# Optimization experiments

Hardware: AMD Instinct MI355X
Metric: run time of the kernel (lower is better)

The kernel has to match this reference:

```python
import jax, jax.numpy as jnp
import numpy as np

N_NODES = 100000
N_EDGES = 1600000
F_IN = 512
HID = 128
N_CLASS = 6


def setup_inputs() -> dict:
    key = jax.random.key(0)
    ks = jax.random.split(key, 12)
    def unif(k, shape, stdv):
        return jax.random.uniform(k, shape, jnp.float32, -stdv, stdv)
    s1 = 1.0 / np.sqrt(HID); s4 = 1.0 / np.sqrt(N_CLASS)
    return {
        "x": jax.random.normal(ks[0], (N_NODES, F_IN), jnp.float32),
        "edge_row": jax.random.randint(ks[1], (N_EDGES,), 0, N_NODES, jnp.int32),
        "edge_col": jax.random.randint(ks[2], (N_EDGES,), 0, N_NODES, jnp.int32),
        "edge_weight": jax.random.uniform(ks[3], (N_EDGES,), jnp.float32),
        "W1": unif(ks[4], (F_IN, HID), s1), "b1": unif(ks[5], (HID,), s1),
        "W2": unif(ks[6], (HID, HID), s1), "b2": unif(ks[7], (HID,), s1),
        "W3": unif(ks[8], (HID, HID), s1), "b3": unif(ks[9], (HID,), s1),
        "W4": unif(ks[10], (HID, N_CLASS), s4), "b4": unif(ks[11], (N_CLASS,), s4),
    }


def _gcn_layer(x, row, col, w_e, W, b):
    # support = x @ W  (dense mm), then spmm(adj, support) in COO form:
    # out[i] = sum_{(i,j) in E} A[i,j] * support[j]
    support = x @ W                              # [N, F_out]
    msgs = support[col] * w_e[:, None]           # [E, F_out] gather + scale
    agg = jax.ops.segment_sum(msgs, row, num_segments=N_NODES)
    return agg + b


def reference(x, edge_row, edge_col, edge_weight, W1, b1, W2, b2, W3, b3, W4, b4):
    # eval mode: F.dropout(training=False) is identity
    h = jax.nn.relu(_gcn_layer(x, edge_row, edge_col, edge_weight, W1, b1))
    h = jax.nn.relu(_gcn_layer(h, edge_row, edge_col, edge_weight, W2, b2))
    h = jax.nn.relu(_gcn_layer(h, edge_row, edge_col, edge_weight, W3, b3))
    return _gcn_layer(h, edge_row, edge_col, edge_weight, W4, b4)
```

## Files before the change

### kernel.cpp

```cpp
#include <hip/hip_runtime.h>
#include <cstdint>

constexpr int NN = 100000;
constexpr int NE = 1600000;
constexpr int FIN = 512;
constexpr int HID = 128;
constexpr int NCLS = 6;
constexpr int EPAD = NE + 3 * NN;

typedef __attribute__((ext_vector_type(8))) short short8v;
typedef __attribute__((ext_vector_type(4))) float f32x4;

constexpr float WINV = 1.0f / 32767.0f;

__device__ __forceinline__ unsigned short f2bf(float f) {
    uint32_t u = __float_as_uint(f);
    uint32_t r = u + 0x7FFFu + ((u >> 16) & 1u);
    return (unsigned short)(r >> 16);
}
__device__ __forceinline__ float bflo(uint32_t u) { return __uint_as_float(u << 16); }
__device__ __forceinline__ float bfhi(uint32_t u) { return __uint_as_float(u & 0xffff0000u); }

__device__ __forceinline__ void gl_lds16(const void* g, void* l) {
    __builtin_amdgcn_global_load_lds(
        (const __attribute__((address_space(1))) unsigned int*)(unsigned long long)g,
        (__attribute__((address_space(3))) unsigned int*)(unsigned int)(unsigned long long)l,
        16, 0, 0);
}

__device__ __forceinline__ void cvt_body(const float* __restrict__ W,
                                         unsigned short* __restrict__ Bp, int t) {
    const int lane = t & 63;
    const int fi = t >> 6;
    const int n = fi & 7, ks = fi >> 3;
    const int krow = ks * 32 + (lane >> 4) * 8;
    const int col = n * 16 + (lane & 15);
    short8v sv;
    #pragma unroll
    for (int j = 0; j < 8; ++j) sv[j] = (short)f2bf(W[(size_t)(krow + j) * HID + col]);
    *(short8v*)&Bp[(size_t)t * 8] = sv;
}

template<int K, bool ABF>
__device__ __forceinline__ void gemm_body(unsigned char* lds,
                                          const void* __restrict__ Av,
                                          const unsigned short* __restrict__ Bp,
                                          unsigned short* __restrict__ C, int bid) {
    constexpr int BM    = 160;
    constexpr int KS    = 32;
    constexpr int EB    = ABF ? 2 : 4;
    constexpr int ROWB  = KS * EB;
    constexpr int SLOTS = ROWB / 16;
    constexpr int SMSK  = SLOTS - 1;
    constexpr int CHUNK = BM * ROWB;
    constexpr int WBYT  = CHUNK / 5;
    constexpr int NISS  = WBYT / 1024;
    constexpr int NS    = K / KS;
    constexpr int WAITN = 8 + NISS;

    const int tid  = threadIdx.x;
    const int lane = tid & 63;
    const int wave = tid >> 6;
    const int row0 = bid * BM;
    const int lr   = lane & 15;
    const int kg   = lane >> 4;

    const unsigned char* Ab = (const unsigned char*)Av;
    const size_t rowbytes = (size_t)K * EB;

    auto stage = [&](int bufsel, int ks) {
        const size_t kbyte = (size_t)ks * ROWB;
        #pragma unroll
        for (int i = 0; i < NISS; ++i) {
            const int Lw   = wave * WBYT + i * 1024 + lane * 16;
            const int row  = Lw / ROWB;
            const int slot = (Lw >> 4) & SMSK;
            const int src  = slot ^ (row & SMSK);
            const unsigned char* g = Ab + (size_t)(row0 + row) * rowbytes + kbyte + src * 16;
            void* l = (void*)&lds[bufsel * CHUNK + wave * WBYT + i * 1024];
            gl_lds16(g, l);
        }
    };

    auto loadB = [&](int ks, short8v (&b)[8]) {
        const unsigned short* bb = Bp + ((size_t)ks * 8 * 64 + lane) * 8;
        #pragma unroll
        for (int n = 0; n < 8; ++n)
            b[n] = *reinterpret_cast<const short8v*>(bb + (size_t)n * 64 * 8);
    };

    short8v bcur[8], bnxt[8];
    f32x4 acc[2][8] = {};

    loadB(0, bcur);
    stage(0, 0);
    asm volatile("s_waitcnt vmcnt(0)" ::: "memory");
    __builtin_amdgcn_sched_barrier(0);

    int cur = 0;
    for (int ks = 0; ks < NS; ++ks) {
        if (ks + 1 < NS) {
            loadB(ks + 1, bnxt);
            stage(cur ^ 1, ks + 1);
            if (ks > 0) {
                asm volatile("s_waitcnt vmcnt(%0)" :: "i"(WAITN) : "memory");
            }
        } else {
            asm volatile("s_waitcnt vmcnt(0)" ::: "memory");
        }
        __builtin_amdgcn_sched_barrier(0);

        const unsigned char* base = &lds[cur * CHUNK];
        const int rA0 = wave * 32 + lr;
        const int rA1 = rA0 + 16;
        const int key = lr & SMSK;

        short8v a0, a1;
        if constexpr (ABF) {
            a0 = *(const short8v*)(base + rA0 * ROWB + ((kg ^ key) * 16));
            a1 = *(const short8v*)(base + rA1 * ROWB + ((kg ^ key) * 16));
        } else {
            const float4 f00 = *(const float4*)(base + rA0 * ROWB + (((2 * kg + 0) ^ key) * 16));
            const float4 f01 = *(const float4*)(base + rA0 * ROWB + (((2 * kg + 1) ^ key) * 16));
            const float4 f10 = *(const float4*)(base + rA1 * ROWB + (((2 * kg + 0) ^ key) * 16));
            const float4 f11 = *(const float4*)(base + rA1 * ROWB + (((2 * kg + 1) ^ key) * 16));
            a0[0] = (short)f2bf(f00.x); a0[1] = (short)f2bf(f00.y);
            a0[2] = (short)f2bf(f00.z); a0[3] = (short)f2bf(f00.w);
            a0[4] = (short)f2bf(f01.x); a0[5] = (short)f2bf(f01.y);
            a0[6] = (short)f2bf(f01.z); a0[7] = (short)f2bf(f01.w);
            a1[0] = (short)f2bf(f10.x); a1[1] = (short)f2bf(f10.y);
            a1[2] = (short)f2bf(f10.z); a1[3] = (short)f2bf(f10.w);
            a1[4] = (short)f2bf(f11.x); a1[5] = (short)f2bf(f11.y);
            a1[6] = (short)f2bf(f11.z); a1[7] = (short)f2bf(f11.w);
        }

        #pragma unroll
        for (int n = 0; n < 8; ++n) {
            acc[0][n] = __builtin_amdgcn_mfma_f32_16x16x32_bf16(a0, bcur[n], acc[0][n], 0, 0, 0);
            acc[1][n] = __builtin_amdgcn_mfma_f32_16x16x32_bf16(a1, bcur[n], acc[1][n], 0, 0, 0);
        }
        if (ks + 1 < NS) {
            #pragma unroll
            for (int n = 0; n < 8; ++n) bcur[n] = bnxt[n];
        }
        cur ^= 1;
    }

    #pragma unroll
    for (int m = 0; m < 2; ++m)
        #pragma unroll
        for (int n = 0; n < 8; ++n)
            #pragma unroll
            for (int i = 0; i < 4; ++i) {
                const int r = row0 + wave * 32 + m * 16 + kg * 4 + i;
                C[(size_t)r * HID + n * 16 + lr] = f2bf(acc[m][n][i]);
            }
}

__launch_bounds__(320)
__global__ void gemm_lds_bf(const void* __restrict__ Av, const unsigned short* __restrict__ Bp,
                            unsigned short* __restrict__ C) {
    __shared__ __attribute__((aligned(16))) unsigned char lds[2 * 160 * 64];
    gemm_body<HID, true>(lds, Av, Bp, C, blockIdx.x);
}

__device__ __forceinline__ void scatter_one(int r, int c, float w,
                                            const int* __restrict__ row_ptr,
                                            int* __restrict__ cur,
                                            uint32_t* __restrict__ edges) {
    const int pos = row_ptr[r] + atomicAdd(&cur[r], 1);
    edges[pos] = ((uint32_t)c << 15) | (uint32_t)(w * 32767.0f + 0.5f);
}

__global__ void fused_hist_cvt(const int4* __restrict__ erow4, int* __restrict__ cnt,
                               const float* __restrict__ W1, const float* __restrict__ W2,
                               const float* __restrict__ W3,
                               unsigned short* __restrict__ Bp1, unsigned short* __restrict__ Bp2,
                               unsigned short* __restrict__ Bp3) {
    constexpr int NB_HIST = (NE / 4 + 255) / 256;
    const int bid = blockIdx.x;
    if (bid < NB_HIST) {
        const int t = bid * 256 + threadIdx.x;
        if (t < NE / 4) {
            const int4 r = erow4[t];
            atomicAdd(&cnt[r.x], 1);
            atomicAdd(&cnt[r.y], 1);
            atomicAdd(&cnt[r.z], 1);
            atomicAdd(&cnt[r.w], 1);
        }
    } else {
        const int t = (bid - NB_HIST) * 256 + threadIdx.x;
        constexpr int T1 = (FIN / 32) * 8 * 64;
        constexpr int T2 = (HID / 32) * 8 * 64;
        if (t < T1)                cvt_body(W1, Bp1, t);
        else if (t < T1 + T2)      cvt_body(W2, Bp2, t - T1);
        else if (t < T1 + 2 * T2)  cvt_body(W3, Bp3, t - T1 - T2);
    }
}

constexpr int GB_GEMM = NN / 160;
constexpr int GB_SCAT = (NE / 4 + 319) / 320;
constexpr int GB_PAD  = (NN + 319) / 320;

__launch_bounds__(320)
__global__ void fused_l1(const float* __restrict__ x, const unsigned short* __restrict__ Bp1,
                         unsigned short* __restrict__ sup16,
                         const int4* __restrict__ erow4, const int4* __restrict__ ecol4,
                         const float4* __restrict__ ew4,
                         const int* __restrict__ row_ptr, const int* __restrict__ row_cnt,
                         int* __restrict__ cur, uint32_t* __restrict__ edges) {
    __shared__ __attribute__((aligned(16))) unsigned char lds[2 * 160 * 128];
    const int bid = blockIdx.x;
    if (bid < GB_GEMM) {
        gemm_body<FIN, false>(lds, x, Bp1, sup16, bid);
    } else if (bid < GB_GEMM + GB_SCAT) {
        const int t = (bid - GB_GEMM) * 320 + threadIdx.x;
        if (t < NE / 4) {
            const int4 r = erow4[t];
            const int4 c = ecol4[t];
            const float4 w = ew4[t];
            scatter_one(r.x, c.x, w.x, row_ptr, cur, edges);
            scatter_one(r.y, c.y, w.y, row_ptr, cur, edges);
            scatter_one(r.z, c.z, w.z, row_ptr, cur, edges);
            scatter_one(r.w, c.w, w.w, row_ptr, cur, edges);
        }
    } else {
        const int r = (bid - GB_GEMM - GB_SCAT) * 320 + threadIdx.x;
        if (r < NN) {
            const int end = row_ptr[r + 1];
            for (int p = row_ptr[r] + row_cnt[r]; p < end; ++p) edges[p] = 0u;
        }
    }
}

__global__ void gemm_w4(const unsigned short* __restrict__ H, const float* __restrict__ W,
                        float* __restrict__ S, int M) {
    __shared__ float Ws[HID * NCLS];
    for (int i = threadIdx.x; i < HID * NCLS; i += blockDim.x) Ws[i] = W[i];
    __syncthreads();
    const int r = blockIdx.x * blockDim.x + threadIdx.x;
    if (r >= M) return;
    float acc[NCLS] = {};
    const unsigned short* h = &H[(size_t)r * HID];
    for (int k0 = 0; k0 < HID; k0 += 8) {
        const uint4 hv = *reinterpret_cast<const uint4*>(&h[k0]);
        float hf[8];
        hf[0] = bflo(hv.x); hf[1] = bfhi(hv.x);
        hf[2] = bflo(hv.y); hf[3] = bfhi(hv.y);
        hf[4] = bflo(hv.z); hf[5] = bfhi(hv.z);
        hf[6] = bflo(hv.w); hf[7] = bfhi(hv.w);
        #pragma unroll
        for (int u = 0; u < 8; ++u)
            #pragma unroll
            for (int j = 0; j < NCLS; ++j)
                acc[j] = fmaf(hf[u], Ws[(k0 + u) * NCLS + j], acc[j]);
    }
    #pragma unroll
    for (int j = 0; j < NCLS; ++j) S[(size_t)r * NCLS + j] = acc[j];
}

__global__ void scan1_k(const int* __restrict__ in, int* __restrict__ out,
                        int* __restrict__ bsum, int n) {
    __shared__ int s[256];
    const int tid = threadIdx.x;
    const int gid = blockIdx.x * 256 + tid;
    const int v = (gid < NN) ? ((in[gid] + 3) & ~3) : 0;
    s[tid] = v;
    __syncthreads();
    for (int off = 1; off < 256; off <<= 1) {
        const int t = (tid >= off) ? s[tid - off] : 0;
        __syncthreads();
        s[tid] += t;
        __syncthreads();
    }
    if (gid < n) out[gid] = s[tid] - v;
    if (tid == 255) bsum[blockIdx.x] = s[255];
}

__global__ void scan2_k(int* __restrict__ bsum, int nb) {
    __shared__ int s[512];
    const int tid = threadIdx.x;
    const int v = (tid < nb) ? bsum[tid] : 0;
    s[tid] = v;
    __syncthreads();
    for (int off = 1; off < 512; off <<= 1) {
        const int t = (tid >= off) ? s[tid - off] : 0;
        __syncthreads();
        s[tid] += t;
        __syncthreads();
    }
    if (tid < nb) bsum[tid] = s[tid] - v;
}

__global__ void scan3_k(int* __restrict__ out, const int* __restrict__ bsum, int n) {
    const int gid = blockIdx.x * 256 + threadIdx.x;
    if (gid < n) out[gid] += bsum[blockIdx.x];
}

template<bool RELU>
__launch_bounds__(256)
__global__ void spmm_bf16(const int* __restrict__ row_ptr,
                          const uint32_t* __restrict__ edges,
                          const unsigned short* __restrict__ S,
                          const float* __restrict__ bias,
                          unsigned short* __restrict__ out) {
    const int lane = threadIdx.x & 63;
    const int row = blockIdx.x * 4 + (threadIdx.x >> 6);
    if (row >= NN) return;
    const int beg = row_ptr[row];
    const int end = row_ptr[row + 1];
    const int fo = lane * 2;
    float2 a0 = *reinterpret_cast<const float2*>(&bias[fo]);
    float2 a1 = {0.f, 0.f}, a2 = {0.f, 0.f}, a3 = {0.f, 0.f};

    int j = beg;
    for (; j + 16 <= end; j += 16) {
        uint4 e0 = *reinterpret_cast<const uint4*>(edges + j);
        uint4 e1 = *reinterpret_cast<const uint4*>(edges + j + 4);
        uint4 e2 = *reinterpret_cast<const uint4*>(edges + j + 8);
        uint4 e3 = *reinterpret_cast<const uint4*>(edges + j + 12);
        const uint32_t ea[16] = {e0.x, e0.y, e0.z, e0.w, e1.x, e1.y, e1.z, e1.w,
                                 e2.x, e2.y, e2.z, e2.w, e3.x, e3.y, e3.z, e3.w};
        uint32_t s[16];
        #pragma unroll
        for (int q = 0; q < 16; ++q)
            s[q] = *reinterpret_cast<const uint32_t*>(&S[(size_t)(ea[q] >> 15) * HID + fo]);
        #pragma unroll
        for (int q = 0; q < 4; ++q) {
            const float w0 = (float)(ea[q]      & 0x7FFFu) * WINV;
            const float w1 = (float)(ea[q + 4]  & 0x7FFFu) * WINV;
            const float w2 = (float)(ea[q + 8]  & 0x7FFFu) * WINV;
            const float w3 = (float)(ea[q + 12] & 0x7FFFu) * WINV;
            a0.x = fmaf(bflo(s[q]),      w0, a0.x); a0.y = fmaf(bfhi(s[q]),      w0, a0.y);
            a1.x = fmaf(bflo(s[q + 4]),  w1, a1.x); a1.y = fmaf(bfhi(s[q + 4]),  w1, a1.y);
            a2.x = fmaf(bflo(s[q + 8]),  w2, a2.x); a2.y = fmaf(bfhi(s[q + 8]),  w2, a2.y);
            a3.x = fmaf(bflo(s[q + 12]), w3, a3.x); a3.y = fmaf(bfhi(s[q + 12]), w3, a3.y);
        }
    }
    for (; j < end; j += 4) {
        const uint4 e = *reinterpret_cast<const uint4*>(edges + j);
        const uint32_t ea[4] = {e.x, e.y, e.z, e.w};
        uint32_t s[4];
        #pragma unroll
        for (int q = 0; q < 4; ++q)
            s[q] = *reinterpret_cast<const uint32_t*>(&S[(size_t)(ea[q] >> 15) * HID + fo]);
        const float w0 = (float)(ea[0] & 0x7FFFu) * WINV;
        const float w1 = (float)(ea[1] & 0x7FFFu) * WINV;
        const float w2 = (float)(ea[2] & 0x7FFFu) * WINV;
        const float w3 = (float)(ea[3] & 0x7FFFu) * WINV;
        a0.x = fmaf(bflo(s[0]), w0, a0.x); a0.y = fmaf(bfhi(s[0]), w0, a0.y);
        a1.x = fmaf(bflo(s[1]), w1, a1.x); a1.y = fmaf(bfhi(s[1]), w1, a1.y);
        a2.x = fmaf(bflo(s[2]), w2, a2.x); a2.y = fmaf(bfhi(s[2]), w2, a2.y);
        a3.x = fmaf(bflo(s[3]), w3, a3.x); a3.y = fmaf(bfhi(s[3]), w3, a3.y);
    }
    float fx = (a0.x + a1.x) + (a2.x + a3.x);
    float fy = (a0.y + a1.y) + (a2.y + a3.y);
    if (RELU) { fx = fmaxf(fx, 0.f); fy = fmaxf(fy, 0.f); }
    const uint32_t o = (uint32_t)f2bf(fx) | ((uint32_t)f2bf(fy) << 16);
    *reinterpret_cast<uint32_t*>(&out[(size_t)row * HID + fo]) = o;
}

__launch_bounds__(256)
__global__ void spmm6(const int* __restrict__ row_ptr,
                      const uint32_t* __restrict__ edges,
                      const float* __restrict__ S,
                      const float* __restrict__ bias,
                      float* __restrict__ out) {
    const int t = blockIdx.x * blockDim.x + threadIdx.x;
    const int row = t >> 4;
    const int sl = t & 15;
    if (row >= NN) return;
    const int beg = row_ptr[row];
    const int end = row_ptr[row + 1];
    float acc[NCLS] = {};
    for (int j = beg + sl; j < end; j += 16) {
        const uint32_t e = edges[j];
        const float w = (float)(e & 0x7FFFu) * WINV;
        const float* s = &S[(size_t)(e >> 15) * NCLS];
        #pragma unroll
        for (int k = 0; k < NCLS; ++k) acc[k] = fmaf(s[k], w, acc[k]);
    }
    #pragma unroll
    for (int off = 8; off > 0; off >>= 1)
        #pragma unroll
        for (int k = 0; k < NCLS; ++k) acc[k] += __shfl_xor(acc[k], off, 64);
    if (sl == 0) {
        #pragma unroll
        for (int k = 0; k < NCLS; ++k) out[(size_t)row * NCLS + k] = acc[k] + bias[k];
    }
}

extern "C" void kernel_launch(void* const* d_in, const int* in_sizes, int n_in,
                              void* d_out, int out_size, void* d_ws, size_t ws_size,
                              hipStream_t stream) {
    const float* x    = (const float*)d_in[0];
    const int*   erow = (const int*)d_in[1];
    const int*   ecol = (const int*)d_in[2];
    const float* ew   = (const float*)d_in[3];
    const float* W1 = (const float*)d_in[4];  const float* b1 = (const float*)d_in[5];
    const float* W2 = (const float*)d_in[6];  const float* b2 = (const float*)d_in[7];
    const float* W3 = (const float*)d_in[8];  const float* b3 = (const float*)d_in[9];
    const float* W4 = (const float*)d_in[10]; const float* b4 = (const float*)d_in[11];
    float* out = (float*)d_out;

    uint32_t*       edges_s = (uint32_t*)d_ws;
    unsigned short* sup16   = (unsigned short*)(edges_s + EPAD);
    unsigned short* h16     = sup16 + (size_t)NN * HID;
    float*          sup6    = (float*)(h16 + (size_t)NN * HID);
    unsigned short* Bp1     = (unsigned short*)(sup6 + (size_t)NN * NCLS);
    unsigned short* Bp2     = Bp1 + (size_t)FIN * HID;
    unsigned short* Bp3     = Bp2 + (size_t)HID * HID;
    int*            row_ptr = (int*)(Bp3 + (size_t)HID * HID);
    int*            row_cnt = row_ptr + (NN + 1);
    int*            row_cur = row_cnt + NN;
    int*            bsum    = row_cur + NN;

    const dim3 blk(256);
    const int  NB = (NN + 1 + 255) / 256;
    constexpr int NB_HIST = (NE / 4 + 255) / 256;
    constexpr int NB_CVT  = 12288 / 256;

    hipMemsetAsync(row_cnt, 0, (size_t)2 * NN * sizeof(int), stream);
    fused_hist_cvt<<<NB_HIST + NB_CVT, blk, 0, stream>>>(
        (const int4*)erow, row_cnt, W1, W2, W3, Bp1, Bp2, Bp3);

    scan1_k<<<NB, blk, 0, stream>>>(row_cnt, row_ptr, bsum, NN + 1);
    scan2_k<<<1, 512, 0, stream>>>(bsum, NB);
    scan3_k<<<NB, blk, 0, stream>>>(row_ptr, bsum, NN + 1);

    fused_l1<<<GB_GEMM + GB_SCAT + GB_PAD, dim3(320), 0, stream>>>(
        x, Bp1, sup16, (const int4*)erow, (const int4*)ecol, (const float4*)ew,
        row_ptr, row_cnt, row_cur, edges_s);

    const int g_spmm = NN / 4;
    spmm_bf16<true><<<g_spmm, blk, 0, stream>>>(row_ptr, edges_s, sup16, b1, h16);
    gemm_lds_bf<<<GB_GEMM, dim3(320), 0, stream>>>(h16, Bp2, sup16);
    spmm_bf16<true><<<g_spmm, blk, 0, stream>>>(row_ptr, edges_s, sup16, b2, h16);
    gemm_lds_bf<<<GB_GEMM, dim3(320), 0, stream>>>(h16, Bp3, sup16);
    spmm_bf16<true><<<g_spmm, blk, 0, stream>>>(row_ptr, edges_s, sup16, b3, h16);
    gemm_w4<<<(NN + 255) / 256, blk, 0, stream>>>(h16, W4, sup6, NN);
    spmm6<<<(NN * 16 + 255) / 256, blk, 0, stream>>>(row_ptr, edges_s, sup6, b4, out);
}
```

Baseline: 413.8 us.

## Co-schedule scatter waves inside GEMM blocks of fused layer-1 kernel

Widens fused_l1 blocks from 320 to 512 threads so each GEMM block carries three extra waves that perform edge scatter and padding work alongside the five GEMM waves. The remaining scatter and pad work is redistributed at wave granularity across a smaller set of extra blocks. This is meant to overlap the memory-bound CSR scatter with the layer-1 GEMM instead of running them in separate blocks, at the cost of larger blocks that may reduce occupancy and contend for resources with the GEMM. It relies on gemm_body not using block-wide barriers that the three extra waves would skip after returning early.

```diff
diff --git a/kernel.cpp b/kernel.cpp
--- a/kernel.cpp
+++ b/kernel.cpp
@@ -199,10 +199,13 @@
 }
 
 constexpr int GB_GEMM = NN / 160;
-constexpr int GB_SCAT = (NE / 4 + 319) / 320;
-constexpr int GB_PAD  = (NN + 319) / 320;
-
-__launch_bounds__(320)
+constexpr int SW_SCAT = NE / 256;
+constexpr int PW_PAD  = (NN + 63) / 64;
+constexpr int TSW     = SW_SCAT + PW_PAD;
+constexpr int GB_XTRA = (TSW - GB_GEMM * 3 + 7) / 8;
+constexpr int GB_TOT  = GB_GEMM + GB_XTRA;
+
+__launch_bounds__(512)
 __global__ void fused_l1(const float* __restrict__ x, const unsigned short* __restrict__ Bp1,
                          unsigned short* __restrict__ sup16,
                          const int4* __restrict__ erow4, const int4* __restrict__ ecol4,
@@ -211,24 +214,29 @@
                          int* __restrict__ cur, uint32_t* __restrict__ edges) {
     __shared__ __attribute__((aligned(16))) unsigned char lds[2 * 160 * 128];
     const int bid = blockIdx.x;
-    if (bid < GB_GEMM) {
+    const int wv  = threadIdx.x >> 6;
+    const int lane = threadIdx.x & 63;
+
+    if (bid < GB_GEMM && wv < 5) {
         gemm_body<FIN, false>(lds, x, Bp1, sup16, bid);
-    } else if (bid < GB_GEMM + GB_SCAT) {
-        const int t = (bid - GB_GEMM) * 320 + threadIdx.x;
-        if (t < NE / 4) {
-            const int4 r = erow4[t];
-            const int4 c = ecol4[t];
-            const float4 w = ew4[t];
-            scatter_one(r.x, c.x, w.x, row_ptr, cur, edges);
-            scatter_one(r.y, c.y, w.y, row_ptr, cur, edges);
-            scatter_one(r.z, c.z, w.z, row_ptr, cur, edges);
-            scatter_one(r.w, c.w, w.w, row_ptr, cur, edges);
-        }
-    } else {
-        const int r = (bid - GB_GEMM - GB_SCAT) * 320 + threadIdx.x;
-        if (r < NN) {
-            const int end = row_ptr[r + 1];
-            for (int p = row_ptr[r] + row_cnt[r]; p < end; ++p) edges[p] = 0u;
+        return;
+    }
+    const int swid = (bid < GB_GEMM) ? bid * 3 + (wv - 5)
+                                     : GB_GEMM * 3 + (bid - GB_GEMM) * 8 + wv;
+    if (swid < SW_SCAT) {
+        const int t = swid * 64 + lane;
+        const int4 r = erow4[t];
+        const int4 c = ecol4[t];
+        const float4 w = ew4[t];
+        scatter_one(r.x, c.x, w.x, row_ptr, cur, edges);
+        scatter_one(r.y, c.y, w.y, row_ptr, cur, edges);
+        scatter_one(r.z, c.z, w.z, row_ptr, cur, edges);
+        scatter_one(r.w, c.w, w.w, row_ptr, cur, edges);
+    } else if (swid < TSW) {
+        const int row = (swid - SW_SCAT) * 64 + lane;
+        if (row < NN) {
+            const int end = row_ptr[row + 1];
+            for (int p = row_ptr[row] + row_cnt[row]; p < end; ++p) edges[p] = 0u;
         }
     }
 }
@@ -420,7 +428,7 @@
     constexpr int NB_HIST = (NE / 4 + 255) / 256;
     constexpr int NB_CVT  = 12288 / 256;
 
-    hipMemsetAsync(row_cnt, 0, (size_t)2 * NN * sizeof(int), stream);
+    (void)hipMemsetAsync(row_cnt, 0, (size_t)2 * NN * sizeof(int), stream);
     fused_hist_cvt<<<NB_HIST + NB_CVT, blk, 0, stream>>>(
         (const int4*)erow, row_cnt, W1, W2, W3, Bp1, Bp2, Bp3);
 
@@ -428,7 +436,7 @@
     scan2_k<<<1, 512, 0, stream>>>(bsum, NB);
     scan3_k<<<NB, blk, 0, stream>>>(row_ptr, bsum, NN + 1);
 
-    fused_l1<<<GB_GEMM + GB_SCAT + GB_PAD, dim3(320), 0, stream>>>(
+    fused_l1<<<GB_TOT, dim3(512), 0, stream>>>(
         x, Bp1, sup16, (const int4*)erow, (const int4*)ecol, (const float4*)ew,
         row_ptr, row_cnt, row_cur, edges_s);
 
```

Measured after the change: 428.0 us. 3.4% more time.
